# Performance work log

Hardware: AMD Instinct MI355X
Metric: run time of the kernel (lower is better)

Reference implementation:

```python
import jax, jax.numpy as jnp
import numpy as np


def setup_inputs() -> dict:
    key = jax.random.key(0)
    ks = jax.random.split(key, 5)
    bsz, input_size, hidden_size, level_hidden = 8192, 1024, 1024, 64
    d_in = input_size + hidden_size
    return {
        "input": jax.random.normal(ks[0], (bsz, input_size), dtype=jnp.float32),
        "h_prev": jax.random.normal(ks[1], (bsz, hidden_size), dtype=jnp.float32),
        "c_prev": jax.random.normal(ks[2], (bsz, hidden_size), dtype=jnp.float32),
        "W_lstm": jax.random.normal(ks[3], (4 * hidden_size, d_in), dtype=jnp.float32) * (1.0 / np.sqrt(d_in)),
        "W_level": jax.random.normal(ks[4], (2 * level_hidden, d_in), dtype=jnp.float32) * (1.0 / np.sqrt(d_in)),
    }


def reference(input, h_prev, c_prev, W_lstm, W_level):
    hidden_size = h_prev.shape[1]
    level_hidden = W_level.shape[0] // 2
    n_repeat = hidden_size // level_hidden

    combined = jnp.concatenate([input, h_prev], axis=-1)  # (B, in+hid)
    lstm_out = combined @ W_lstm.T                        # (B, 4*hid)
    cc_i, cc_f, cc_o, cc_g = jnp.split(lstm_out, 4, axis=1)
    level_out = combined @ W_level.T                      # (B, 2*lvl)
    cc_i_h, cc_f_h = jnp.split(level_out, 2, axis=1)

    i = jax.nn.sigmoid(cc_i)
    f = jax.nn.sigmoid(cc_f)
    o = jax.nn.sigmoid(cc_o)
    g = jnp.tanh(cc_g)

    p_f = jax.nn.softmax(cc_f_h, axis=-1)
    p_i = jax.nn.softmax(cc_i_h, axis=-1)
    f_h = jnp.cumsum(p_f, axis=-1)                         # forward cumsum
    i_h = jnp.flip(jnp.cumsum(jnp.flip(p_i, -1), axis=-1), -1)  # reverse cumsum

    # expand each level gate value across its chunk of the hidden dim
    i_h = jnp.repeat(i_h, n_repeat, axis=1)                # (B, hid)
    f_h = jnp.repeat(f_h, n_repeat, axis=1)

    w = i_h * f_h
    c = w * (f * c_prev + i * g) + (f_h - w) * c_prev + (i_h - w) * g
    h = o * jnp.tanh(c)
    return (h, c)
```

## Files before the change

kernel.cpp:

```cpp
#include <hip/hip_runtime.h>


typedef unsigned short u16;
typedef __attribute__((ext_vector_type(8))) short bf16x8;
typedef __attribute__((ext_vector_type(8))) short s8v;
typedef __attribute__((ext_vector_type(4))) float f32x4;
typedef __attribute__((ext_vector_type(4))) float v4f;

#define GLDS(g, l) __builtin_amdgcn_global_load_lds(                      \
    (const __attribute__((address_space(1))) void*)(g),                   \
    (__attribute__((address_space(3))) void*)(l), 16, 0, 0)

__device__ __forceinline__ u16 f2bf(float x) {
  unsigned u = __builtin_bit_cast(unsigned, x);
  u += 0x7FFFu + ((u >> 16) & 1u);
  return (u16)(u >> 16);
}
__device__ __forceinline__ float bf2f(u16 h) {
  unsigned u = ((unsigned)h) << 16;
  return __builtin_bit_cast(float, u);
}
__device__ __forceinline__ float fsig(float x) { return 1.0f / (1.0f + __expf(-x)); }
__device__ __forceinline__ float ftanhf(float x) { float e = __expf(2.0f * x); return 1.0f - 2.0f / (e + 1.0f); }

__global__ __launch_bounds__(256) void k_convert(
    const float* __restrict__ inp, const float* __restrict__ hprev,
    const float* __restrict__ wl, const float* __restrict__ wlev,
    u16* __restrict__ Ahi, u16* __restrict__ Whi, u16* __restrict__ Wlo)
{
  const int GA = (8192 * 2048) / 8;
  const int GW = (4224 * 2048) / 8;
  for (int gi = blockIdx.x * 256 + threadIdx.x; gi < GA + GW; gi += gridDim.x * 256) {
    if (gi < GA) {
      int e = gi << 3; int row = e >> 11, col = e & 2047;
      const float* src = (col < 1024) ? (inp + row * 1024 + col)
                                      : (hprev + row * 1024 + (col - 1024));
      v4f a = *(const v4f*)src, b = *(const v4f*)(src + 4);
      float vv[8] = {a.x, a.y, a.z, a.w, b.x, b.y, b.z, b.w};
      s8v hi;
#pragma unroll
      for (int j = 0; j < 8; ++j) hi[j] = (short)f2bf(vv[j]);
      *(s8v*)(Ahi + e) = hi;
    } else {
      int e = (gi - GA) << 3; int n = e >> 11, k = e & 2047;
      const float* src;
      if (n < 4096) { int j = n >> 2, g = n & 3; src = wl + (size_t)((g << 10) | j) * 2048 + k; }
      else          { src = wlev + (size_t)(n - 4096) * 2048 + k; }
      v4f a = *(const v4f*)src, b = *(const v4f*)(src + 4);
      float vv[8] = {a.x, a.y, a.z, a.w, b.x, b.y, b.z, b.w};
      s8v hi, lo;
#pragma unroll
      for (int j = 0; j < 8; ++j) {
        u16 h = f2bf(vv[j]);
        hi[j] = (short)h;
        lo[j] = (short)f2bf(vv[j] - bf2f(h));
      }
      *(s8v*)(Whi + e) = hi;
      if (n >= 4096) *(s8v*)(Wlo + (size_t)(n - 4096) * 2048 + k) = lo;
    }
  }
}

__global__ __launch_bounds__(256) void k_level_fused(
    const u16* __restrict__ Ahi, const u16* __restrict__ Whi,
    const u16* __restrict__ Wlo, float* __restrict__ ih, float* __restrict__ fh)
{
  __shared__ __align__(16) u16 smem[2 * 18432];
  const int tid = threadIdx.x, lane = tid & 63, wid = tid >> 6;
  const int c16 = lane & 15, r16 = lane >> 4;
  const int r0 = blockIdx.x << 5;

  const int row_t = tid >> 3;
  const int xk8 = ((tid & 7) ^ (row_t & 7)) << 3;
  const u16* pa_s  = Ahi + (size_t)(r0 + row_t) * 2048 + xk8;
  const u16* pbh_s = Whi + (size_t)(4096 + row_t) * 2048 + xk8;
  const u16* pbl_s = Wlo + (size_t)row_t * 2048 + xk8;
  char* const ldsW = (char*)smem + (wid << 10);

  const int sl0 = ((r16 ^ (c16 & 7)) << 3);
  const int sl1 = (((4 | r16) ^ (c16 & 7)) << 3);

  f32x4 acc[2][2] = {};

#define LSTAGE(kt, buf) do {                                           \
    char* d_ = ldsW + (buf) * 36864;                                   \
    const int ko_ = (kt) * 64;                                         \
    GLDS(pa_s + ko_, d_);                                              \
    GLDS(pbh_s + ko_,          d_ + 4096);                             \
    GLDS(pbh_s + ko_ + 65536,  d_ + 8192);                             \
    GLDS(pbh_s + ko_ + 131072, d_ + 12288);                            \
    GLDS(pbh_s + ko_ + 196608, d_ + 16384);                            \
    GLDS(pbl_s + ko_,          d_ + 20480);                            \
    GLDS(pbl_s + ko_ + 65536,  d_ + 24576);                            \
    GLDS(pbl_s + ko_ + 131072, d_ + 28672);                            \
    GLDS(pbl_s + ko_ + 196608, d_ + 32768);                            \
  } while (0)

#define LCOMP(buf) do {                                                \
    const u16* bp_ = smem + (buf) * 18432;                             \
    _Pragma("unroll")                                                  \
    for (int ks = 0; ks < 2; ++ks) {                                   \
      const int sx_ = ks ? sl1 : sl0;                                  \
      bf16x8 ah[2];                                                    \
      _Pragma("unroll")                                                \
      for (int mi = 0; mi < 2; ++mi)                                   \
        ah[mi] = *(const bf16x8*)(bp_ + (mi * 16 + c16) * 64 + sx_);   \
      _Pragma("unroll")                                                \
      for (int j = 0; j < 2; ++j) {                                    \
        int br_ = (wid * 32 + j * 16 + c16) * 64 + sx_;                \
        bf16x8 bh = *(const bf16x8*)(bp_ + 2048 + br_);                \
        bf16x8 bl = *(const bf16x8*)(bp_ + 10240 + br_);               \
        _Pragma("unroll")                                              \
        for (int mi = 0; mi < 2; ++mi) {                               \
          acc[mi][j] = __builtin_amdgcn_mfma_f32_16x16x32_bf16(ah[mi], bh, acc[mi][j], 0, 0, 0); \
          acc[mi][j] = __builtin_amdgcn_mfma_f32_16x16x32_bf16(ah[mi], bl, acc[mi][j], 0, 0, 0); \
        }                                                              \
      }                                                                \
    }                                                                  \
  } while (0)

#define LTILE(t, buf, dostage) do {                                    \
    if (dostage) LSTAGE((t) + 1, (buf) ^ 1);                           \
    if (dostage) asm volatile("s_waitcnt vmcnt(9)" ::: "memory");      \
    else         asm volatile("s_waitcnt vmcnt(0)" ::: "memory");      \
    __builtin_amdgcn_s_barrier();                                      \
    LCOMP(buf);                                                        \
    __builtin_amdgcn_s_barrier();                                      \
  } while (0)

  LSTAGE(0, 0);
  for (int u = 0; u < 15; ++u) {
    LTILE(2 * u, 0, 1);
    LTILE(2 * u + 1, 1, 1);
  }
  LTILE(30, 0, 1);
  LTILE(31, 1, 0);
#undef LTILE
#undef LCOMP
#undef LSTAGE

  float* epi = (float*)smem;
#pragma unroll
  for (int mi = 0; mi < 2; ++mi)
#pragma unroll
    for (int j = 0; j < 2; ++j)
#pragma unroll
      for (int r = 0; r < 4; ++r)
        epi[(mi * 16 + r16 * 4 + r) * 128 + wid * 32 + j * 16 + c16] = acc[mi][j][r];
  __syncthreads();

  for (int rr = 0; rr < 8; ++rr) {
    int row = wid * 8 + rr;
    float vi = epi[row * 128 + lane];
    float vf = epi[row * 128 + 64 + lane];
    float mi = vi, mf = vf;
#pragma unroll
    for (int d = 1; d < 64; d <<= 1) {
      mi = fmaxf(mi, __shfl_xor(mi, d, 64));
      mf = fmaxf(mf, __shfl_xor(mf, d, 64));
    }
    float ei = __expf(vi - mi), ef = __expf(vf - mf);
    float si = ei, sf = ef;
#pragma unroll
    for (int d = 1; d < 64; d <<= 1) {
      si += __shfl_xor(si, d, 64);
      sf += __shfl_xor(sf, d, 64);
    }
    float pi = ei / si, pf = ef / sf;
    float ci = pi, cf = pf;
#pragma unroll
    for (int d = 1; d < 64; d <<= 1) {
      float t = __shfl_up(ci, d, 64); if (lane >= d) ci += t;
      float uu = __shfl_up(cf, d, 64); if (lane >= d) cf += uu;
    }
    int rowg = r0 + row;
    ih[(rowg << 6) + lane] = 1.0f - (ci - pi);
    fh[(rowg << 6) + lane] = cf;
  }
}

__global__ __launch_bounds__(512, 4) void k_gemm_main(
    const u16* __restrict__ Ab, const u16* __restrict__ Wb,
    const float* __restrict__ cprev, const float* __restrict__ ihp,
    const float* __restrict__ fhp, float* __restrict__ out)
{
  __shared__ __align__(16) u16 smem[36864];
  const int tid = threadIdx.x, lane = tid & 63, wid = tid >> 6;
  const int wm = wid >> 1, wn = wid & 1;
  const int c16 = lane & 15, r16 = lane >> 4;

  const int bx = blockIdx.x;
  const int nb = (bx & 7) * 128 + (bx >> 3);
  const int rm = nb >> 5, cm = nb & 31;

  const int sr = tid >> 2;
  const int slq = tid & 3;
  const int xk = (slq ^ ((sr >> 1) & 3)) << 3;
  const u16* pa = Ab + (size_t)(rm * 256 + sr) * 2048 + xk;
  const u16* pb = Wb + (size_t)(cm * 128 + sr) * 2048 + xk;
  char* const ldsW = (char*)smem + (wid << 10);

  const int xsl = (r16 ^ ((c16 >> 1) & 3)) << 3;
  const int base_a = (wm * 64 + c16) * 32 + xsl;
  const int base_b = 8192 + (wn * 64 + c16) * 32 + xsl;

  f32x4 acc[4][4] = {};

#define STAGE3(slice, slot) do {                                       \
    const u16* sa_ = pa + (slice) * 32;                                \
    const u16* sb_ = pb + (slice) * 32;                                \
    char* d_ = ldsW + (slot) * 24576;                                  \
    GLDS(sa_, d_); GLDS(sa_ + 262144, d_ + 8192);                      \
    GLDS(sb_, d_ + 16384);                                             \
  } while (0)

#define SLICE(s, slot, dostage) do {                                   \
    bf16x8 aX[4], bS[4];                                               \
    _Pragma("unroll")                                                  \
    for (int i = 0; i < 4; ++i)                                        \
      aX[i] = *(const bf16x8*)(smem + (slot) * 12288 + base_a + i * 512); \
    _Pragma("unroll")                                                  \
    for (int j = 0; j < 4; ++j)                                        \
      bS[j] = *(const bf16x8*)(smem + (slot) * 12288 + base_b + j * 512); \
    if (dostage) STAGE3(((s) + 2) & 63, ((s) + 2) % 3);                \
    asm volatile("s_waitcnt vmcnt(3)" ::: "memory");                   \
    __builtin_amdgcn_s_barrier();                                      \
    asm volatile("s_waitcnt lgkmcnt(0)" ::: "memory");                 \
    _Pragma("unroll")                                                  \
    for (int i = 0; i < 4; ++i)                                        \
      _Pragma("unroll")                                                \
      for (int j = 0; j < 4; ++j)                                      \
        acc[i][j] = __builtin_amdgcn_mfma_f32_16x16x32_bf16(           \
            aX[i], bS[j], acc[i][j], 0, 0, 0);                         \
    __builtin_amdgcn_s_barrier();                                      \
  } while (0)

  STAGE3(0, 0); STAGE3(1, 1);
  asm volatile("s_waitcnt vmcnt(3)" ::: "memory");
  __builtin_amdgcn_s_barrier();

  for (int u = 0; u < 21; ++u) {
    const int s0 = u * 3;
    SLICE(s0 + 0, 0, 1);
    SLICE(s0 + 1, 1, 1);
    SLICE(s0 + 2, 2, 1);
  }
  SLICE(63, 0, 0);
#undef SLICE
#undef STAGE3

  asm volatile("s_waitcnt vmcnt(0)" ::: "memory");
  __builtin_amdgcn_s_barrier();

  float* epi = (float*)smem;
#define EPIPASS(p) do {                                                \
    if ((wm >> 1) == (p)) {                                            \
      _Pragma("unroll")                                                \
      for (int i = 0; i < 4; ++i)                                      \
        _Pragma("unroll")                                              \
        for (int j = 0; j < 4; ++j)                                    \
          _Pragma("unroll")                                            \
          for (int r = 0; r < 4; ++r) {                                \
            float v = acc[i][j][r];                                    \
            v = ((c16 & 3) == 3) ? ftanhf(v) : fsig(v);                \
            epi[((wm & 1) * 64 + i * 16 + r16 * 4 + r) * 128 +         \
                wn * 64 + j * 16 + c16] = v;                           \
          }                                                            \
    }                                                                  \
    __syncthreads();                                                   \
    _Pragma("unroll")                                                  \
    for (int e = 0; e < 2; ++e) {                                      \
      int idx = (e << 9) + tid;                                        \
      int mrow = idx >> 3, q = idx & 7;                                \
      const float* g4 = epi + mrow * 128 + q * 16;                     \
      int rowg = rm * 256 + (p) * 128 + mrow;                          \
      int jgb = cm * 32 + q * 4;                                       \
      int lv = jgb >> 4;                                               \
      float vih = ihp[(rowg << 6) + lv], vfh = fhp[(rowg << 6) + lv];  \
      float wq = vih * vfh;                                            \
      v4f cp4 = *(const v4f*)(cprev + rowg * 1024 + jgb);              \
      float cpv[4] = {cp4.x, cp4.y, cp4.z, cp4.w};                     \
      v4f hv, cv;                                                      \
      _Pragma("unroll")                                                \
      for (int t = 0; t < 4; ++t) {                                    \
        v4f g = *(const v4f*)(g4 + t * 4);                             \
        float iv = g.x, fv = g.y, ov = g.z, gv = g.w;                  \
        float cpx = cpv[t];                                            \
        float c = wq * (fv * cpx + iv * gv) + (vfh - wq) * cpx + (vih - wq) * gv; \
        float h = ov * ftanhf(c);                                      \
        hv[t] = h; cv[t] = c;                                          \
      }                                                                \
      *(v4f*)(out + rowg * 1024 + jgb) = hv;                           \
      *(v4f*)(out + 8388608 + rowg * 1024 + jgb) = cv;                 \
    }                                                                  \
    __syncthreads();                                                   \
  } while (0)
  EPIPASS(0); EPIPASS(1);
#undef EPIPASS
}

extern "C" void kernel_launch(void* const* d_in, const int* in_sizes, int n_in,
                              void* d_out, int out_size, void* d_ws, size_t ws_size,
                              hipStream_t stream) {
  (void)in_sizes; (void)n_in; (void)out_size; (void)ws_size;
  const float* inp   = (const float*)d_in[0];
  const float* hprev = (const float*)d_in[1];
  const float* cprev = (const float*)d_in[2];
  const float* wl    = (const float*)d_in[3];
  const float* wlev  = (const float*)d_in[4];
  float* out = (float*)d_out;
  char* ws = (char*)d_ws;

  u16* Ahi  = (u16*)(ws);
  u16* Whi  = (u16*)(ws + 67108864);
  u16* Wlo  = (u16*)(ws + 84410368);
  float* ih   = (float*)(ws + 118489088);
  float* fh   = (float*)(ws + 120586240);

  k_convert<<<dim3(2048), dim3(256), 0, stream>>>(inp, hprev, wl, wlev, Ahi, Whi, Wlo);
  k_level_fused<<<dim3(256), dim3(256), 0, stream>>>(Ahi, Whi, Wlo, ih, fh);
  k_gemm_main<<<dim3(1024), dim3(512), 0, stream>>>(Ahi, Whi, cprev, ih, fh, out);
}
```

Baseline: 203.6 us.

## Shrink GEMM tile to 128x128 with 4-stage LDS ring and one barrier per slice

The main GEMM block drops from 512 threads on a 256x128 tile to 256 threads on a 128x128 tile, with twice as many blocks and a remapped block swizzle. The LDS pipeline goes from a 3-slot to a 4-slot ring, which lets each slice use one barrier instead of two, and the tail drains with explicit vmcnt(0) waits. The epilogue becomes a single pass because the smaller tile fits in shared memory at once. The aim is less barrier stall and better occupancy and latency hiding, at the cost of lower A/B reuse per block and more total global loads.

```diff
diff --git a/kernel.cpp b/kernel.cpp
--- a/kernel.cpp
+++ b/kernel.cpp
@@ -179,51 +179,55 @@
   }
 }
 
-__global__ __launch_bounds__(512, 4) void k_gemm_main(
+__global__ __launch_bounds__(256, 2) void k_gemm_main(
     const u16* __restrict__ Ab, const u16* __restrict__ Wb,
     const float* __restrict__ cprev, const float* __restrict__ ihp,
     const float* __restrict__ fhp, float* __restrict__ out)
 {
-  __shared__ __align__(16) u16 smem[36864];
+  __shared__ __align__(16) u16 smem[32768];
   const int tid = threadIdx.x, lane = tid & 63, wid = tid >> 6;
   const int wm = wid >> 1, wn = wid & 1;
   const int c16 = lane & 15, r16 = lane >> 4;
 
   const int bx = blockIdx.x;
-  const int nb = (bx & 7) * 128 + (bx >> 3);
+  const int nb = (bx & 7) * 256 + (bx >> 3);
   const int rm = nb >> 5, cm = nb & 31;
 
   const int sr = tid >> 2;
   const int slq = tid & 3;
   const int xk = (slq ^ ((sr >> 1) & 3)) << 3;
-  const u16* pa = Ab + (size_t)(rm * 256 + sr) * 2048 + xk;
+  const u16* pa = Ab + (size_t)(rm * 128 + sr) * 2048 + xk;
   const u16* pb = Wb + (size_t)(cm * 128 + sr) * 2048 + xk;
   char* const ldsW = (char*)smem + (wid << 10);
 
   const int xsl = (r16 ^ ((c16 >> 1) & 3)) << 3;
   const int base_a = (wm * 64 + c16) * 32 + xsl;
-  const int base_b = 8192 + (wn * 64 + c16) * 32 + xsl;
+  const int base_b = 4096 + (wn * 64 + c16) * 32 + xsl;
 
   f32x4 acc[4][4] = {};
 
-#define STAGE3(slice, slot) do {                                       \
+#define STAGE4(slice, slot) do {                                       \
     const u16* sa_ = pa + (slice) * 32;                                \
     const u16* sb_ = pb + (slice) * 32;                                \
-    char* d_ = ldsW + (slot) * 24576;                                  \
-    GLDS(sa_, d_); GLDS(sa_ + 262144, d_ + 8192);                      \
-    GLDS(sb_, d_ + 16384);                                             \
+    char* d_ = ldsW + (slot) * 16384;                                  \
+    GLDS(sa_, d_);           GLDS(sa_ + 131072, d_ + 4096);            \
+    GLDS(sb_, d_ + 8192);    GLDS(sb_ + 131072, d_ + 12288);           \
   } while (0)
 
 #define SLICE(s, slot, dostage) do {                                   \
     bf16x8 aX[4], bS[4];                                               \
     _Pragma("unroll")                                                  \
     for (int i = 0; i < 4; ++i)                                        \
-      aX[i] = *(const bf16x8*)(smem + (slot) * 12288 + base_a + i * 512); \
+      aX[i] = *(const bf16x8*)(smem + (slot) * 8192 + base_a + i * 512); \
     _Pragma("unroll")                                                  \
     for (int j = 0; j < 4; ++j)                                        \
-      bS[j] = *(const bf16x8*)(smem + (slot) * 12288 + base_b + j * 512); \
-    if (dostage) STAGE3(((s) + 2) & 63, ((s) + 2) % 3);                \
-    asm volatile("s_waitcnt vmcnt(3)" ::: "memory");                   \
+      bS[j] = *(const bf16x8*)(smem + (slot) * 8192 + base_b + j * 512); \
+    if (dostage) {                                                     \
+      STAGE4(((s) + 2) & 63, ((s) + 2) & 3);                           \
+      asm volatile("s_waitcnt vmcnt(4)" ::: "memory");                 \
+    } else {                                                           \
+      asm volatile("s_waitcnt vmcnt(0)" ::: "memory");                 \
+    }                                                                  \
     __builtin_amdgcn_s_barrier();                                      \
     asm volatile("s_waitcnt lgkmcnt(0)" ::: "memory");                 \
     _Pragma("unroll")                                                  \
@@ -232,71 +236,65 @@
       for (int j = 0; j < 4; ++j)                                      \
         acc[i][j] = __builtin_amdgcn_mfma_f32_16x16x32_bf16(           \
             aX[i], bS[j], acc[i][j], 0, 0, 0);                         \
-    __builtin_amdgcn_s_barrier();                                      \
-  } while (0)
-
-  STAGE3(0, 0); STAGE3(1, 1);
-  asm volatile("s_waitcnt vmcnt(3)" ::: "memory");
+  } while (0)
+
+  STAGE4(0, 0); STAGE4(1, 1);
+  asm volatile("s_waitcnt vmcnt(4)" ::: "memory");
   __builtin_amdgcn_s_barrier();
 
-  for (int u = 0; u < 21; ++u) {
-    const int s0 = u * 3;
+  for (int u = 0; u < 15; ++u) {
+    const int s0 = u * 4;
     SLICE(s0 + 0, 0, 1);
     SLICE(s0 + 1, 1, 1);
     SLICE(s0 + 2, 2, 1);
-  }
-  SLICE(63, 0, 0);
+    SLICE(s0 + 3, 3, 1);
+  }
+  SLICE(60, 0, 1);
+  SLICE(61, 1, 1);
+  SLICE(62, 2, 0);
+  SLICE(63, 3, 0);
 #undef SLICE
-#undef STAGE3
-
-  asm volatile("s_waitcnt vmcnt(0)" ::: "memory");
+#undef STAGE4
+
   __builtin_amdgcn_s_barrier();
 
   float* epi = (float*)smem;
-#define EPIPASS(p) do {                                                \
-    if ((wm >> 1) == (p)) {                                            \
-      _Pragma("unroll")                                                \
-      for (int i = 0; i < 4; ++i)                                      \
-        _Pragma("unroll")                                              \
-        for (int j = 0; j < 4; ++j)                                    \
-          _Pragma("unroll")                                            \
-          for (int r = 0; r < 4; ++r) {                                \
-            float v = acc[i][j][r];                                    \
-            v = ((c16 & 3) == 3) ? ftanhf(v) : fsig(v);                \
-            epi[((wm & 1) * 64 + i * 16 + r16 * 4 + r) * 128 +         \
-                wn * 64 + j * 16 + c16] = v;                           \
-          }                                                            \
-    }                                                                  \
-    __syncthreads();                                                   \
-    _Pragma("unroll")                                                  \
-    for (int e = 0; e < 2; ++e) {                                      \
-      int idx = (e << 9) + tid;                                        \
-      int mrow = idx >> 3, q = idx & 7;                                \
-      const float* g4 = epi + mrow * 128 + q * 16;                     \
-      int rowg = rm * 256 + (p) * 128 + mrow;                          \
-      int jgb = cm * 32 + q * 4;                                       \
-      int lv = jgb >> 4;                                               \
-      float vih = ihp[(rowg << 6) + lv], vfh = fhp[(rowg << 6) + lv];  \
-      float wq = vih * vfh;                                            \
-      v4f cp4 = *(const v4f*)(cprev + rowg * 1024 + jgb);              \
-      float cpv[4] = {cp4.x, cp4.y, cp4.z, cp4.w};                     \
-      v4f hv, cv;                                                      \
-      _Pragma("unroll")                                                \
-      for (int t = 0; t < 4; ++t) {                                    \
-        v4f g = *(const v4f*)(g4 + t * 4);                             \
-        float iv = g.x, fv = g.y, ov = g.z, gv = g.w;                  \
-        float cpx = cpv[t];                                            \
-        float c = wq * (fv * cpx + iv * gv) + (vfh - wq) * cpx + (vih - wq) * gv; \
-        float h = ov * ftanhf(c);                                      \
-        hv[t] = h; cv[t] = c;                                          \
-      }                                                                \
-      *(v4f*)(out + rowg * 1024 + jgb) = hv;                           \
-      *(v4f*)(out + 8388608 + rowg * 1024 + jgb) = cv;                 \
-    }                                                                  \
-    __syncthreads();                                                   \
-  } while (0)
-  EPIPASS(0); EPIPASS(1);
-#undef EPIPASS
+#pragma unroll
+  for (int i = 0; i < 4; ++i)
+#pragma unroll
+    for (int j = 0; j < 4; ++j)
+#pragma unroll
+      for (int r = 0; r < 4; ++r) {
+        float v = acc[i][j][r];
+        v = ((c16 & 3) == 3) ? ftanhf(v) : fsig(v);
+        epi[(wm * 64 + i * 16 + r16 * 4 + r) * 128 + wn * 64 + j * 16 + c16] = v;
+      }
+  __syncthreads();
+#pragma unroll
+  for (int e = 0; e < 4; ++e) {
+    int idx = (e << 8) + tid;
+    int mrow = idx >> 3, q = idx & 7;
+    const float* g4 = epi + mrow * 128 + q * 16;
+    int rowg = rm * 128 + mrow;
+    int jgb = cm * 32 + q * 4;
+    int lv = jgb >> 4;
+    float vih = ihp[(rowg << 6) + lv], vfh = fhp[(rowg << 6) + lv];
+    float wq = vih * vfh;
+    v4f cp4 = *(const v4f*)(cprev + rowg * 1024 + jgb);
+    float cpv[4] = {cp4.x, cp4.y, cp4.z, cp4.w};
+    v4f hv, cv;
+#pragma unroll
+    for (int t = 0; t < 4; ++t) {
+      v4f g = *(const v4f*)(g4 + t * 4);
+      float iv = g.x, fv = g.y, ov = g.z, gv = g.w;
+      float cpx = cpv[t];
+      float c = wq * (fv * cpx + iv * gv) + (vfh - wq) * cpx + (vih - wq) * gv;
+      float h = ov * ftanhf(c);
+      hv[t] = h; cv[t] = c;
+    }
+    *(v4f*)(out + rowg * 1024 + jgb) = hv;
+    *(v4f*)(out + 8388608 + rowg * 1024 + jgb) = cv;
+  }
 }
 
 extern "C" void kernel_launch(void* const* d_in, const int* in_sizes, int n_in,
@@ -319,5 +317,5 @@
 
   k_convert<<<dim3(2048), dim3(256), 0, stream>>>(inp, hprev, wl, wlev, Ahi, Whi, Wlo);
   k_level_fused<<<dim3(256), dim3(256), 0, stream>>>(Ahi, Whi, Wlo, ih, fh);
-  k_gemm_main<<<dim3(1024), dim3(512), 0, stream>>>(Ahi, Whi, cprev, ih, fh, out);
-}
+  k_gemm_main<<<dim3(2048), dim3(256), 0, stream>>>(Ahi, Whi, cprev, ih, fh, out);
+}
```

New measurement: 229.9 us. 12.9% more time.

## Enlarge GEMM block tile to 256x256 with 8x4 MFMA accumulators per wave

Applied to the files above, without the earlier changes.

Doubles the N extent of each workgroup's output tile from 128 to 256 columns, so each wave computes 128x64 instead of 64x64. The LDS stage grows to hold a 256-row B slice, the epilogue runs four passes, and the grid halves to 512 blocks. The aim is better operand reuse per byte loaded from global memory and LDS. The cost is higher register pressure (launch bounds relaxed to 2 blocks/CU), larger LDS, and fewer blocks to spread across CUs.

```diff
diff --git a/kernel.cpp b/kernel.cpp
--- a/kernel.cpp
+++ b/kernel.cpp
@@ -179,55 +179,55 @@
   }
 }
 
-__global__ __launch_bounds__(512, 4) void k_gemm_main(
+__global__ __launch_bounds__(512, 2) void k_gemm_main(
     const u16* __restrict__ Ab, const u16* __restrict__ Wb,
     const float* __restrict__ cprev, const float* __restrict__ ihp,
     const float* __restrict__ fhp, float* __restrict__ out)
 {
-  __shared__ __align__(16) u16 smem[36864];
+  __shared__ __align__(16) u16 smem[49152];
   const int tid = threadIdx.x, lane = tid & 63, wid = tid >> 6;
-  const int wm = wid >> 1, wn = wid & 1;
+  const int wm = wid >> 2, wn = wid & 3;
   const int c16 = lane & 15, r16 = lane >> 4;
 
   const int bx = blockIdx.x;
-  const int nb = (bx & 7) * 128 + (bx >> 3);
-  const int rm = nb >> 5, cm = nb & 31;
+  const int nb = (bx & 7) * 64 + (bx >> 3);
+  const int rm = nb >> 4, cm = nb & 15;
 
   const int sr = tid >> 2;
   const int slq = tid & 3;
   const int xk = (slq ^ ((sr >> 1) & 3)) << 3;
   const u16* pa = Ab + (size_t)(rm * 256 + sr) * 2048 + xk;
-  const u16* pb = Wb + (size_t)(cm * 128 + sr) * 2048 + xk;
+  const u16* pb = Wb + (size_t)(cm * 256 + sr) * 2048 + xk;
   char* const ldsW = (char*)smem + (wid << 10);
 
   const int xsl = (r16 ^ ((c16 >> 1) & 3)) << 3;
-  const int base_a = (wm * 64 + c16) * 32 + xsl;
-  const int base_b = 8192 + (wn * 64 + c16) * 32 + xsl;
-
-  f32x4 acc[4][4] = {};
-
-#define STAGE3(slice, slot) do {                                       \
+  const int base_a = wm * 4096 + c16 * 32 + xsl;
+  const int base_b = 8192 + (wn >> 1) * 4096 + ((wn & 1) * 64 + c16) * 32 + xsl;
+
+  f32x4 acc[8][4] = {};
+
+#define STAGE4(slice, slot) do {                                       \
     const u16* sa_ = pa + (slice) * 32;                                \
     const u16* sb_ = pb + (slice) * 32;                                \
-    char* d_ = ldsW + (slot) * 24576;                                  \
-    GLDS(sa_, d_); GLDS(sa_ + 262144, d_ + 8192);                      \
-    GLDS(sb_, d_ + 16384);                                             \
+    char* d_ = ldsW + (slot) * 32768;                                  \
+    GLDS(sa_, d_);           GLDS(sa_ + 262144, d_ + 8192);            \
+    GLDS(sb_, d_ + 16384);   GLDS(sb_ + 262144, d_ + 24576);           \
   } while (0)
 
 #define SLICE(s, slot, dostage) do {                                   \
-    bf16x8 aX[4], bS[4];                                               \
-    _Pragma("unroll")                                                  \
-    for (int i = 0; i < 4; ++i)                                        \
-      aX[i] = *(const bf16x8*)(smem + (slot) * 12288 + base_a + i * 512); \
+    bf16x8 aX[8], bS[4];                                               \
+    _Pragma("unroll")                                                  \
+    for (int i = 0; i < 8; ++i)                                        \
+      aX[i] = *(const bf16x8*)(smem + (slot) * 16384 + base_a + i * 512); \
     _Pragma("unroll")                                                  \
     for (int j = 0; j < 4; ++j)                                        \
-      bS[j] = *(const bf16x8*)(smem + (slot) * 12288 + base_b + j * 512); \
-    if (dostage) STAGE3(((s) + 2) & 63, ((s) + 2) % 3);                \
-    asm volatile("s_waitcnt vmcnt(3)" ::: "memory");                   \
+      bS[j] = *(const bf16x8*)(smem + (slot) * 16384 + base_b + j * 512); \
+    if (dostage) STAGE4(((s) + 2) & 63, ((s) + 2) % 3);                \
+    asm volatile("s_waitcnt vmcnt(4)" ::: "memory");                   \
     __builtin_amdgcn_s_barrier();                                      \
     asm volatile("s_waitcnt lgkmcnt(0)" ::: "memory");                 \
     _Pragma("unroll")                                                  \
-    for (int i = 0; i < 4; ++i)                                        \
+    for (int i = 0; i < 8; ++i)                                        \
       _Pragma("unroll")                                                \
       for (int j = 0; j < 4; ++j)                                      \
         acc[i][j] = __builtin_amdgcn_mfma_f32_16x16x32_bf16(           \
@@ -235,8 +235,8 @@
     __builtin_amdgcn_s_barrier();                                      \
   } while (0)
 
-  STAGE3(0, 0); STAGE3(1, 1);
-  asm volatile("s_waitcnt vmcnt(3)" ::: "memory");
+  STAGE4(0, 0); STAGE4(1, 1);
+  asm volatile("s_waitcnt vmcnt(4)" ::: "memory");
   __builtin_amdgcn_s_barrier();
 
   for (int u = 0; u < 21; ++u) {
@@ -247,34 +247,33 @@
   }
   SLICE(63, 0, 0);
 #undef SLICE
-#undef STAGE3
+#undef STAGE4
 
   asm volatile("s_waitcnt vmcnt(0)" ::: "memory");
   __builtin_amdgcn_s_barrier();
 
   float* epi = (float*)smem;
 #define EPIPASS(p) do {                                                \
-    if ((wm >> 1) == (p)) {                                            \
-      _Pragma("unroll")                                                \
-      for (int i = 0; i < 4; ++i)                                      \
+    if (wm == ((p) >> 1)) {                                            \
+      _Pragma("unroll")                                                \
+      for (int iq = 0; iq < 4; ++iq)                                   \
         _Pragma("unroll")                                              \
         for (int j = 0; j < 4; ++j)                                    \
           _Pragma("unroll")                                            \
           for (int r = 0; r < 4; ++r) {                                \
-            float v = acc[i][j][r];                                    \
+            float v = acc[((p) & 1) * 4 + iq][j][r];                   \
             v = ((c16 & 3) == 3) ? ftanhf(v) : fsig(v);                \
-            epi[((wm & 1) * 64 + i * 16 + r16 * 4 + r) * 128 +         \
-                wn * 64 + j * 16 + c16] = v;                           \
+            epi[(iq * 16 + r16 * 4 + r) * 256 + wn * 64 + j * 16 + c16] = v; \
           }                                                            \
     }                                                                  \
     __syncthreads();                                                   \
     _Pragma("unroll")                                                  \
     for (int e = 0; e < 2; ++e) {                                      \
       int idx = (e << 9) + tid;                                        \
-      int mrow = idx >> 3, q = idx & 7;                                \
-      const float* g4 = epi + mrow * 128 + q * 16;                     \
-      int rowg = rm * 256 + (p) * 128 + mrow;                          \
-      int jgb = cm * 32 + q * 4;                                       \
+      int m = idx >> 4, q = idx & 15;                                  \
+      const float* g4 = epi + m * 256 + q * 16;                        \
+      int rowg = rm * 256 + (p) * 64 + m;                              \
+      int jgb = cm * 64 + q * 4;                                       \
       int lv = jgb >> 4;                                               \
       float vih = ihp[(rowg << 6) + lv], vfh = fhp[(rowg << 6) + lv];  \
       float wq = vih * vfh;                                            \
@@ -295,7 +294,7 @@
     }                                                                  \
     __syncthreads();                                                   \
   } while (0)
-  EPIPASS(0); EPIPASS(1);
+  EPIPASS(0); EPIPASS(1); EPIPASS(2); EPIPASS(3);
 #undef EPIPASS
 }
 
@@ -319,5 +318,5 @@
 
   k_convert<<<dim3(2048), dim3(256), 0, stream>>>(inp, hprev, wl, wlev, Ahi, Whi, Wlo);
   k_level_fused<<<dim3(256), dim3(256), 0, stream>>>(Ahi, Whi, Wlo, ih, fh);
-  k_gemm_main<<<dim3(1024), dim3(512), 0, stream>>>(Ahi, Whi, cprev, ih, fh, out);
-}
+  k_gemm_main<<<dim3(512), dim3(512), 0, stream>>>(Ahi, Whi, cprev, ih, fh, out);
+}
```

Result: slower. 208.3 us (+2.3%).
